# Kernel tuning notes

Hardware: AMD Instinct MI355X
Metric: run time of the kernel (lower is better)

## Reference

```python
import jax, jax.numpy as jnp
import numpy as np

ALPHA = 0.2          # LeakyReLU negative slope
NEG_INF = -9e15      # mask value from the original code


def setup_inputs() -> dict:
    key = jax.random.key(0)
    k1, k2, k3, k4 = jax.random.split(key, 4)
    B, N, F_in, F_out = 8, 2048, 64, 64
    x = jax.random.normal(k1, (B, N, F_in), dtype=jnp.float32)
    adj = jax.random.randint(k2, (B, N, N), 0, 2, dtype=jnp.int32)
    W = jax.random.normal(k3, (F_in, F_out), dtype=jnp.float32)
    a = jax.random.normal(k4, (2 * F_out, 1), dtype=jnp.float32)
    return {"x": x, "adj": adj, "W": W, "a": a}


def reference(x, adj, W, a):
    # h: [B, N, F_out]
    h = jnp.matmul(x, W)
    F_out = W.shape[1]
    a1 = a[:F_out, 0]   # source half of attention vector
    a2 = a[F_out:, 0]   # target half
    # e_ij = leakyrelu(h_i . a1 + h_j . a2)  -- identical math to the
    # original cat([h_i, h_j]) @ a without materializing [B,N*N,2F].
    s1 = jnp.einsum('bnf,f->bn', h, a1)  # [B, N]
    s2 = jnp.einsum('bnf,f->bn', h, a2)  # [B, N]
    e = jax.nn.leaky_relu(s1[:, :, None] + s2[:, None, :], negative_slope=ALPHA)
    masked = jnp.where(adj > 0, e, NEG_INF)
    attention = jax.nn.softmax(masked, axis=2)  # [B, N, N]
    # dropout p=0.0 / eval mode -> identity
    h_prime = jnp.matmul(attention, h)          # [B, N, F_out]
    return jax.nn.elu(h_prime)                  # concat=True branch
```

## Files before the change

kernel.cpp:

```cpp
#include <hip/hip_runtime.h>
#include <cstdint>

#define LRELU_ALPHA 0.2f
#define NEG_INF -9000000000000000.0f
#define L2E 1.4426950408889634f

typedef __bf16 bf16x8 __attribute__((ext_vector_type(8)));
typedef float floatx4 __attribute__((ext_vector_type(4)));

constexpr int Bb = 8, Nn = 2048, Ff = 64;
constexpr int TJ = 64;
constexpr int SEG = 8;
constexpr int SEGJ = Nn / SEG;
constexpr int SEGT = SEGJ / TJ;
constexpr int NROWS = Bb * Nn;
constexpr int LSTR = 264;

__device__ __forceinline__ unsigned f2bf_u(float f) {
    unsigned u = __builtin_bit_cast(unsigned, f);
    return u + 0x7FFFu + ((u >> 16) & 1u);
}

__device__ __forceinline__ unsigned short f2bf(float f) {
    return (unsigned short)(f2bf_u(f) >> 16);
}

__device__ __forceinline__ unsigned pkbf(float lo, float hi) {
    return (f2bf_u(lo) >> 16) | (f2bf_u(hi) & 0xFFFF0000u);
}

__global__ __launch_bounds__(256) void gat_prep(
    const float* __restrict__ x, const float* __restrict__ W, const float* __restrict__ a,
    unsigned short* __restrict__ hT, float* __restrict__ s1g, float* __restrict__ s2g)
{
    constexpr int STR2 = 36;
    __shared__ unsigned short hblk[64 * STR2];
    const int tid = threadIdx.x;
    const int blk = blockIdx.x;
    const int b  = blk >> 6;
    const int i0 = (blk & 63) * 32;
    const int w    = tid >> 6;
    const int lane = tid & 63;

    float wcol[64];
    #pragma unroll
    for (int k = 0; k < 64; ++k) wcol[k] = W[k * 64 + lane];
    const float a1 = a[lane], a2 = a[64 + lane];

    for (int r = 0; r < 8; ++r) {
        const int il = w * 8 + r;
        const int i  = i0 + il;
        const float* xrow = x + ((size_t)(b * Nn + i)) * 64;
        float h = 0.f;
        #pragma unroll
        for (int k = 0; k < 64; ++k) h = fmaf(xrow[k], wcol[k], h);
        float p1 = h * a1, p2 = h * a2;
        #pragma unroll
        for (int off = 32; off; off >>= 1) {
            p1 += __shfl_xor(p1, off);
            p2 += __shfl_xor(p2, off);
        }
        if (lane == 0) { s1g[b * Nn + i] = p1 * L2E; s2g[b * Nn + i] = p2 * L2E; }
        hblk[lane * STR2 + il] = f2bf(h);
    }
    __syncthreads();
    {
        const int f = tid >> 2, c = (tid & 3) * 8;
        uint4 v = *reinterpret_cast<const uint4*>(&hblk[f * STR2 + c]);
        *reinterpret_cast<uint4*>(hT + ((size_t)b * 64 + f) * Nn + i0 + c) = v;
    }
}

__global__ __launch_bounds__(256, 4) void gat_attn(
    const int* __restrict__ adj, const unsigned short* __restrict__ hT,
    const float* __restrict__ s1g, const float* __restrict__ s2g,
    float* __restrict__ m_part, float* __restrict__ l_part, float* __restrict__ O_part)
{
    __shared__ unsigned short hT_lds[64 * LSTR];
    __shared__ float s2_lds[SEGJ];

    const int tid  = threadIdx.x;
    const int blk  = blockIdx.x;
    const int seg  = blk >> 8;
    const int grp  = blk & 255;
    const int gr0  = grp * 64;
    const int b    = gr0 >> 11;
    const int i0   = gr0 & 2047;
    const int w    = tid >> 6;
    const int lane = tid & 63;
    const int fl   = lane & 15;
    const int q    = lane >> 4;

    const int i = i0 + w * 16 + fl;
    const float s1v = s1g[b * Nn + i];
    const int* adj_row = adj + ((size_t)(b * Nn + i)) * Nn;
    const unsigned short* hTb = hT + (size_t)b * 64 * Nn;
    const int jseg0 = seg * SEGJ;

    float m = NEG_INF, l = 0.f;
    floatx4 C[4] = {};

    auto loadAdj = [&](int4* dst, int jcol0) {
        const int* p0 = adj_row + jcol0 + q * 8;
        dst[0] = *reinterpret_cast<const int4*>(p0);
        dst[1] = *reinterpret_cast<const int4*>(p0 + 4);
        const int* p1 = adj_row + jcol0 + 32 + q * 8;
        dst[2] = *reinterpret_cast<const int4*>(p1);
        dst[3] = *reinterpret_cast<const int4*>(p1 + 4);
    };

    int4 bufA[4], bufB[4];
    loadAdj(bufA, jseg0);
    loadAdj(bufB, jseg0 + TJ);

    {
        const int fr = tid >> 2;
        const int c0 = (tid & 3) * 64;
        const unsigned short* gsrc = hTb + (size_t)fr * Nn + jseg0 + c0;
        #pragma unroll
        for (int k = 0; k < 8; ++k) {
            uint4 v = reinterpret_cast<const uint4*>(gsrc)[k];
            reinterpret_cast<uint4*>(&hT_lds[fr * LSTR + c0])[k] = v;
        }
        s2_lds[tid] = s2g[b * Nn + jseg0 + tid];
    }
    __syncthreads();

    auto tile_body = [&](const int4* av4, int tloc) {
        const int* av = reinterpret_cast<const int*>(av4);
        float e[16];
        #pragma unroll
        for (int t = 0; t < 2; ++t) {
            float s2v[8];
            *reinterpret_cast<float4*>(&s2v[0]) =
                *reinterpret_cast<const float4*>(&s2_lds[tloc * 64 + t * 32 + q * 8]);
            *reinterpret_cast<float4*>(&s2v[4]) =
                *reinterpret_cast<const float4*>(&s2_lds[tloc * 64 + t * 32 + q * 8 + 4]);
            #pragma unroll
            for (int jj = 0; jj < 8; ++jj) {
                float ev = s1v + s2v[jj];
                ev = fmaxf(ev, LRELU_ALPHA * ev);
                e[t * 8 + jj] = (av[t * 8 + jj] > 0) ? ev : NEG_INF;
            }
        }
        float tmax = e[0];
        #pragma unroll
        for (int k = 1; k < 16; ++k) tmax = fmaxf(tmax, e[k]);
        tmax = fmaxf(tmax, __shfl_xor(tmax, 16));
        tmax = fmaxf(tmax, __shfl_xor(tmax, 32));
        const float m_new = fmaxf(m, tmax);
        const float alpha_s = exp2f(m - m_new);
        m = m_new;

        float tsum = 0.f, p[16];
        #pragma unroll
        for (int k = 0; k < 16; ++k) {
            p[k] = exp2f(e[k] - m_new);
            tsum += p[k];
        }
        tsum += __shfl_xor(tsum, 16);
        tsum += __shfl_xor(tsum, 32);
        l = l * alpha_s + tsum;

        uint4 pl0, pl1;
        pl0.x = pkbf(p[0], p[1]);  pl0.y = pkbf(p[2], p[3]);
        pl0.z = pkbf(p[4], p[5]);  pl0.w = pkbf(p[6], p[7]);
        pl1.x = pkbf(p[8], p[9]);  pl1.y = pkbf(p[10], p[11]);
        pl1.z = pkbf(p[12], p[13]); pl1.w = pkbf(p[14], p[15]);
        const bf16x8 A0 = __builtin_bit_cast(bf16x8, pl0);
        const bf16x8 A1 = __builtin_bit_cast(bf16x8, pl1);

        float ac[4];
        #pragma unroll
        for (int r = 0; r < 4; ++r) ac[r] = __shfl(alpha_s, q * 4 + r);
        #pragma unroll
        for (int u = 0; u < 4; ++u)
            #pragma unroll
            for (int r = 0; r < 4; ++r) C[u][r] *= ac[r];

        #pragma unroll
        for (int u = 0; u < 4; ++u) {
            const bf16x8 B0 = *reinterpret_cast<const bf16x8*>(
                &hT_lds[(u * 16 + fl) * LSTR + tloc * 64 + q * 8]);
            C[u] = __builtin_amdgcn_mfma_f32_16x16x32_bf16(A0, B0, C[u], 0, 0, 0);
            const bf16x8 B1 = *reinterpret_cast<const bf16x8*>(
                &hT_lds[(u * 16 + fl) * LSTR + tloc * 64 + 32 + q * 8]);
            C[u] = __builtin_amdgcn_mfma_f32_16x16x32_bf16(A1, B1, C[u], 0, 0, 0);
        }
    };

    tile_body(bufA, 0);
    loadAdj(bufA, jseg0 + 2 * TJ);
    tile_body(bufB, 1);
    loadAdj(bufB, jseg0 + 3 * TJ);
    tile_body(bufA, 2);
    tile_body(bufB, 3);

    if (q == 0) {
        const int ri = b * Nn + i;
        m_part[seg * NROWS + ri] = m;
        l_part[seg * NROWS + ri] = l;
    }
    #pragma unroll
    for (int u = 0; u < 4; ++u) {
        #pragma unroll
        for (int r = 0; r < 4; ++r) {
            const int orow = i0 + w * 16 + q * 4 + r;
            O_part[((size_t)seg * NROWS + b * Nn + orow) * 64 + u * 16 + fl] = C[u][r];
        }
    }
}

__global__ __launch_bounds__(256) void gat_merge(
    const float* __restrict__ m_part, const float* __restrict__ l_part,
    const float* __restrict__ O_part, float* __restrict__ out)
{
    const int tid = threadIdx.x;
    const int ri  = blockIdx.x * 4 + (tid >> 6);
    const int f   = tid & 63;

    float mv[SEG];
    #pragma unroll
    for (int s = 0; s < SEG; ++s) mv[s] = m_part[s * NROWS + ri];
    float mstar = mv[0];
    #pragma unroll
    for (int s = 1; s < SEG; ++s) mstar = fmaxf(mstar, mv[s]);

    float lsum = 0.f, acc = 0.f;
    #pragma unroll
    for (int s = 0; s < SEG; ++s) {
        const float wgt = exp2f(mv[s] - mstar);
        lsum += l_part[s * NROWS + ri] * wgt;
        acc  += O_part[((size_t)s * NROWS + ri) * 64 + f] * wgt;
    }
    float v = acc / lsum;
    v = (v > 0.f) ? v : (exp2f(v * L2E) - 1.f);
    out[(size_t)ri * 64 + f] = v;
}

extern "C" void kernel_launch(void* const* d_in, const int* in_sizes, int n_in,
                              void* d_out, int out_size, void* d_ws, size_t ws_size,
                              hipStream_t stream) {
    const float* x   = (const float*)d_in[0];
    const int*   adj = (const int*)d_in[1];
    const float* W   = (const float*)d_in[2];
    const float* a   = (const float*)d_in[3];
    float* out = (float*)d_out;

    char* p = (char*)d_ws;
    unsigned short* hT = (unsigned short*)p;  p += (size_t)Bb * 64 * Nn * sizeof(unsigned short);
    float* s1 = (float*)p;                    p += (size_t)NROWS * sizeof(float);
    float* s2 = (float*)p;                    p += (size_t)NROWS * sizeof(float);
    float* m_part = (float*)p;                p += (size_t)SEG * NROWS * sizeof(float);
    float* l_part = (float*)p;                p += (size_t)SEG * NROWS * sizeof(float);
    float* O_part = (float*)p;

    gat_prep<<<dim3(Bb * Nn / 32), dim3(256), 0, stream>>>(x, W, a, hT, s1, s2);
    gat_attn<<<dim3(SEG * (Bb * Nn / 64)), dim3(256), 0, stream>>>(
        adj, hT, s1, s2, m_part, l_part, O_part);
    gat_merge<<<dim3(NROWS / 4), dim3(256), 0, stream>>>(m_part, l_part, O_part, out);
}
```

Baseline: 238.0 us.

## Pre-pack adjacency into bitmasks with coalesced ballot kernel before attention

```diff
diff --git a/kernel.cpp b/kernel.cpp
--- a/kernel.cpp
+++ b/kernel.cpp
@@ -12,7 +12,6 @@
 constexpr int TJ = 64;
 constexpr int SEG = 8;
 constexpr int SEGJ = Nn / SEG;
-constexpr int SEGT = SEGJ / TJ;
 constexpr int NROWS = Bb * Nn;
 constexpr int LSTR = 264;
 
@@ -20,13 +19,34 @@
     unsigned u = __builtin_bit_cast(unsigned, f);
     return u + 0x7FFFu + ((u >> 16) & 1u);
 }
-
 __device__ __forceinline__ unsigned short f2bf(float f) {
     return (unsigned short)(f2bf_u(f) >> 16);
 }
-
 __device__ __forceinline__ unsigned pkbf(float lo, float hi) {
     return (f2bf_u(lo) >> 16) | (f2bf_u(hi) & 0xFFFF0000u);
+}
+
+__global__ __launch_bounds__(256) void gat_pack(
+    const int* __restrict__ adj, unsigned long long* __restrict__ amask)
+{
+    const int lane = threadIdx.x & 63;
+    const int w    = threadIdx.x >> 6;
+    const long long wave_id = (long long)blockIdx.x * 4 + w;
+    const long long c0 = wave_id * 16;
+    #pragma unroll
+    for (int it = 0; it < 16; ++it) {
+        const long long chunk = c0 + it;
+        const int4 v = reinterpret_cast<const int4*>(adj + chunk * 256)[lane];
+        const unsigned long long b0 = __ballot(v.x > 0);
+        const unsigned long long b1 = __ballot(v.y > 0);
+        const unsigned long long b2 = __ballot(v.z > 0);
+        const unsigned long long b3 = __ballot(v.w > 0);
+        if (lane == 0) {
+            ulonglong2* o = reinterpret_cast<ulonglong2*>(amask + chunk * 4);
+            o[0] = ulonglong2{b0, b1};
+            o[1] = ulonglong2{b2, b3};
+        }
+    }
 }
 
 __global__ __launch_bounds__(256) void gat_prep(
@@ -72,7 +92,7 @@
 }
 
 __global__ __launch_bounds__(256, 4) void gat_attn(
-    const int* __restrict__ adj, const unsigned short* __restrict__ hT,
+    const unsigned long long* __restrict__ amask, const unsigned short* __restrict__ hT,
     const float* __restrict__ s1g, const float* __restrict__ s2g,
     float* __restrict__ m_part, float* __restrict__ l_part, float* __restrict__ O_part)
 {
@@ -93,25 +113,19 @@
 
     const int i = i0 + w * 16 + fl;
     const float s1v = s1g[b * Nn + i];
-    const int* adj_row = adj + ((size_t)(b * Nn + i)) * Nn;
     const unsigned short* hTb = hT + (size_t)b * 64 * Nn;
     const int jseg0 = seg * SEGJ;
 
+    unsigned long long Bw0, Bw1, Bw2, Bw3;
+    {
+        const unsigned long long* mrow = amask + (((size_t)(b * Nn + i)) * 8 + seg) * 4;
+        ulonglong2 m01 = reinterpret_cast<const ulonglong2*>(mrow)[0];
+        ulonglong2 m23 = reinterpret_cast<const ulonglong2*>(mrow)[1];
+        Bw0 = m01.x; Bw1 = m01.y; Bw2 = m23.x; Bw3 = m23.y;
+    }
+
     float m = NEG_INF, l = 0.f;
     floatx4 C[4] = {};
-
-    auto loadAdj = [&](int4* dst, int jcol0) {
-        const int* p0 = adj_row + jcol0 + q * 8;
-        dst[0] = *reinterpret_cast<const int4*>(p0);
-        dst[1] = *reinterpret_cast<const int4*>(p0 + 4);
-        const int* p1 = adj_row + jcol0 + 32 + q * 8;
-        dst[2] = *reinterpret_cast<const int4*>(p1);
-        dst[3] = *reinterpret_cast<const int4*>(p1 + 4);
-    };
-
-    int4 bufA[4], bufB[4];
-    loadAdj(bufA, jseg0);
-    loadAdj(bufB, jseg0 + TJ);
 
     {
         const int fr = tid >> 2;
@@ -126,8 +140,15 @@
     }
     __syncthreads();
 
-    auto tile_body = [&](const int4* av4, int tloc) {
-        const int* av = reinterpret_cast<const int*>(av4);
+    const int q2 = q * 2;
+
+    auto tile_body = [&](int tloc) {
+        unsigned w32[4];
+        w32[0] = (unsigned)(Bw0 >> (tloc * 16 + q2));
+        w32[1] = (unsigned)(Bw1 >> (tloc * 16 + q2));
+        w32[2] = (unsigned)(Bw2 >> (tloc * 16 + q2));
+        w32[3] = (unsigned)(Bw3 >> (tloc * 16 + q2));
+
         float e[16];
         #pragma unroll
         for (int t = 0; t < 2; ++t) {
@@ -140,7 +161,8 @@
             for (int jj = 0; jj < 8; ++jj) {
                 float ev = s1v + s2v[jj];
                 ev = fmaxf(ev, LRELU_ALPHA * ev);
-                e[t * 8 + jj] = (av[t * 8 + jj] > 0) ? ev : NEG_INF;
+                const bool on = (w32[jj & 3] >> (t * 8 + (jj >> 2))) & 1u;
+                e[t * 8 + jj] = on ? ev : NEG_INF;
             }
         }
         float tmax = e[0];
@@ -189,12 +211,10 @@
         }
     };
 
-    tile_body(bufA, 0);
-    loadAdj(bufA, jseg0 + 2 * TJ);
-    tile_body(bufB, 1);
-    loadAdj(bufB, jseg0 + 3 * TJ);
-    tile_body(bufA, 2);
-    tile_body(bufB, 3);
+    tile_body(0);
+    tile_body(1);
+    tile_body(2);
+    tile_body(3);
 
     if (q == 0) {
         const int ri = b * Nn + i;
@@ -253,10 +273,12 @@
     float* s2 = (float*)p;                    p += (size_t)NROWS * sizeof(float);
     float* m_part = (float*)p;                p += (size_t)SEG * NROWS * sizeof(float);
     float* l_part = (float*)p;                p += (size_t)SEG * NROWS * sizeof(float);
-    float* O_part = (float*)p;
-
+    float* O_part = (float*)p;                p += (size_t)SEG * NROWS * 64 * sizeof(float);
+    unsigned long long* amask = (unsigned long long*)p;
+
+    gat_pack<<<dim3(2048), dim3(256), 0, stream>>>(adj, amask);
     gat_prep<<<dim3(Bb * Nn / 32), dim3(256), 0, stream>>>(x, W, a, hT, s1, s2);
     gat_attn<<<dim3(SEG * (Bb * Nn / 64)), dim3(256), 0, stream>>>(
-        adj, hT, s1, s2, m_part, l_part, O_part);
+        amask, hT, s1, s2, m_part, l_part, O_part);
     gat_merge<<<dim3(NROWS / 4), dim3(256), 0, stream>>>(m_part, l_part, O_part, out);
 }
```

Result: slower. 247.7 us (+4.1%).
